# Kernel optimization log

Hardware: AMD Instinct MI355X
Metric: run time of the kernel (lower is better)

The kernel has to match this reference:

```python
import jax, jax.numpy as jnp
import numpy as np
from jax import lax

EPS = 1e-12  # tf.nn.l2_normalize epsilon


def setup_inputs() -> dict:
    key = jax.random.key(0)
    k1, k2, k3 = jax.random.split(key, 3)
    B, T, D, C, F, K = 64, 2048, 1024, 1024, 256, 5
    sentence_embed = jax.random.normal(k1, (B, T, D), dtype=jnp.float32)
    label_embed = jax.random.normal(k2, (C, D), dtype=jnp.float32)
    conv_w = jax.random.normal(k3, (K, C, F), dtype=jnp.float32) * 0.05
    conv_b = jnp.zeros((F,), dtype=jnp.float32)
    return {"sentence_embed": sentence_embed, "label_embed": label_embed,
            "conv_w": conv_w, "conv_b": conv_b}


def reference(sentence_embed, label_embed, conv_w, conv_b):
    # l2-normalize label embeddings along feature dim (tf.nn.l2_normalize semantics)
    sq = jnp.sum(label_embed * label_embed, axis=-1, keepdims=True)
    label_norm = label_embed * lax.rsqrt(jnp.maximum(sq, EPS))
    # G: [B, T, C] = sentence_embed @ label_norm^T (raw sentence_embed, per original)
    G = jnp.einsum('btd,cd->btc', sentence_embed, label_norm)
    # Conv1D over time, 'same' padding, relu: [B, T, F]
    conv = lax.conv_general_dilated(
        G, conv_w, window_strides=(1,), padding='SAME',
        dimension_numbers=('NWC', 'WIO', 'NWC'))
    conv = jax.nn.relu(conv + conv_b)
    # max over filters -> attention values [B, T] (NOT softmaxed in original output path)
    att_v = jnp.max(conv, axis=-1)
    # batch_dot(sentence_embed, att_v, axes=[1,1]) -> [B, D]
    H_enc = jnp.einsum('btd,bt->bd', sentence_embed, att_v)
    return H_enc
```

## Files before the change

kernel.cpp:

```cpp
#include <hip/hip_runtime.h>

typedef unsigned short u16;
typedef __attribute__((ext_vector_type(4))) float f32x4;
typedef __attribute__((ext_vector_type(8))) short s16x8;
typedef __attribute__((ext_vector_type(4))) unsigned short u16x4;

#define DEV __device__ __forceinline__

constexpr int Bb = 64, Tt = 2048, Dd = 1024, Cc = 1024, Ff = 256;
constexpr int TP = Tt + 4;
constexpr int M1 = Bb * Tt;

DEV u16 f2bf(float f) {
    union { float f; unsigned u; } v; v.f = f;
    unsigned r = v.u + 0x7fffu + ((v.u >> 16) & 1u);
    return (u16)(r >> 16);
}
DEV float bf2f(u16 h) {
    union { unsigned u; float f; } v; v.u = ((unsigned)h) << 16; return v.f;
}

DEV void gl_lds16(const u16* g, u16* l) {
    __builtin_amdgcn_global_load_lds(
        (const __attribute__((address_space(1))) unsigned*)(const void*)g,
        (__attribute__((address_space(3))) unsigned*)(void*)l,
        16, 0, 0);
}

DEV int swz_scol(int lane) { return (((lane & 7) ^ ((lane >> 3) & 7)) << 3); }
DEV int swz_rd(int row, int e) { return e ^ ((row & 7) << 3); }

__global__ __launch_bounds__(256) void k_s2bf(const float* __restrict__ S,
                                              u16* __restrict__ Sb) {
    size_t i = ((size_t)blockIdx.x * 256 + threadIdx.x) * 8;
    const size_t stride = (size_t)gridDim.x * 256 * 8;
    const size_t n = (size_t)M1 * Dd;
    for (; i < n; i += stride) {
        f32x4 a = *(const f32x4*)(S + i);
        f32x4 b = *(const f32x4*)(S + i + 4);
        s16x8 r;
        r[0] = (short)f2bf(a.x); r[1] = (short)f2bf(a.y);
        r[2] = (short)f2bf(a.z); r[3] = (short)f2bf(a.w);
        r[4] = (short)f2bf(b.x); r[5] = (short)f2bf(b.y);
        r[6] = (short)f2bf(b.z); r[7] = (short)f2bf(b.w);
        *(s16x8*)(Sb + i) = r;
    }
}

__global__ __launch_bounds__(256) void k_label_norm(const float* __restrict__ L,
                                                    u16* __restrict__ Ln) {
    int c = blockIdx.x;
    int t = threadIdx.x;
    const float* row = L + (size_t)c * Dd;
    float s = 0.f;
    for (int d = t; d < Dd; d += 256) { float v = row[d]; s += v * v; }
    for (int o = 32; o; o >>= 1) s += __shfl_down(s, o);
    __shared__ float red[4];
    if ((t & 63) == 0) red[t >> 6] = s;
    __syncthreads();
    float tot = red[0] + red[1] + red[2] + red[3];
    float r = rsqrtf(fmaxf(tot, 1e-12f));
    for (int d = t; d < Dd; d += 256) Ln[(size_t)c * Dd + d] = f2bf(row[d] * r);
}

__global__ __launch_bounds__(256) void k_wt(const float* __restrict__ W,
                                            u16* __restrict__ Wt) {
    __shared__ float tile[64][65];
    int k = blockIdx.x; int c0 = blockIdx.y * 64; int f0 = blockIdx.z * 64;
    int tid = threadIdx.x;
    const float* Wk = W + (size_t)k * Cc * Ff;
    #pragma unroll
    for (int i = 0; i < 16; ++i) {
        int q = tid + i * 256;
        int ci = q >> 6, fj = q & 63;
        tile[ci][fj] = Wk[(size_t)(c0 + ci) * Ff + f0 + fj];
    }
    __syncthreads();
    #pragma unroll
    for (int i = 0; i < 16; ++i) {
        int q = tid + i * 256;
        int fi = q >> 6, cj = q & 63;
        Wt[((size_t)k * Ff + f0 + fi) * Cc + c0 + cj] = f2bf(tile[cj][fi]);
    }
}

__global__ __launch_bounds__(256) void k_zpad(u16* __restrict__ Gp) {
    int b_ = blockIdx.x, tid = threadIdx.x;
    size_t base = (size_t)b_ * TP * Cc;
    for (int i = tid; i < 2 * Cc; i += 256) {
        Gp[base + i] = 0;
        Gp[base + (size_t)(TP - 2) * Cc + i] = 0;
    }
}

__global__ __launch_bounds__(512, 2) void k_gemm1_8ph(const u16* __restrict__ Sb,
                                                      const u16* __restrict__ Ln,
                                                      u16* __restrict__ Gp) {
    __shared__ alignas(16) u16 As[2][256 * 64];
    __shared__ alignas(16) u16 Bs[2][256 * 64];
    int bid = blockIdx.x;
    int xcd = bid & 7, idx = bid >> 3;
    int mt = xcd * 64 + (idx >> 2);
    int nt = idx & 3;
    const int m0 = mt * 256, n0 = nt * 256;
    int tid = threadIdx.x, lane = tid & 63, wid = tid >> 6;
    int wm = wid >> 2, wn = wid & 3;
    int srow = lane >> 3, scol = swz_scol(lane);
    const int rsel = lane & 15;
    const int klo = (lane >> 4) * 8, khi = 32 + klo;
    f32x4 acc[8][4] = {};

    auto stageA = [&](int kt, int h, int buf) {
        #pragma unroll
        for (int i = 0; i < 2; ++i) {
            int seg = h * 16 + wid * 2 + i;
            gl_lds16(Sb + (size_t)(m0 + seg * 8 + srow) * Dd + kt * 64 + scol,
                     &As[buf][seg * 512]);
        }
    };
    auto stageB = [&](int kt, int h, int buf) {
        #pragma unroll
        for (int i = 0; i < 2; ++i) {
            int seg = h * 16 + wid * 2 + i;
            gl_lds16(Ln + (size_t)(n0 + seg * 8 + srow) * Dd + kt * 64 + scol,
                     &Bs[buf][seg * 512]);
        }
    };

    stageA(0, 0, 0); stageA(0, 1, 0);
    stageB(0, 0, 0); stageB(0, 1, 0);
    asm volatile("s_waitcnt vmcnt(0)" ::: "memory");
    asm volatile("s_barrier" ::: "memory");

    for (int kt = 0; kt < 16; ++kt) {
        const int cur = kt & 1, nxt = cur ^ 1;
        const u16* Ab = As[cur];
        const u16* Bq = Bs[cur];
        s16x8 a[4], b[4];
        #pragma unroll
        for (int f = 0; f < 4; ++f) {
            int row = wm * 128 + f * 16 + rsel;
            a[f] = *(const s16x8*)&Ab[row * 64 + swz_rd(row, klo)];
        }
        #pragma unroll
        for (int f = 0; f < 4; ++f) {
            int row = wn * 64 + f * 16 + rsel;
            b[f] = *(const s16x8*)&Bq[row * 64 + swz_rd(row, klo)];
        }
        if (kt < 15) { stageA(kt + 1, 0, nxt); stageB(kt + 1, 0, nxt); }
        __builtin_amdgcn_s_barrier();
        __builtin_amdgcn_s_setprio(1);
        #pragma unroll
        for (int fm = 0; fm < 4; ++fm)
            #pragma unroll
            for (int fn = 0; fn < 4; ++fn)
                acc[fm][fn] = __builtin_amdgcn_mfma_f32_16x16x32_bf16(
                    a[fm], b[fn], acc[fm][fn], 0, 0, 0);
        __builtin_amdgcn_s_setprio(0);
        __builtin_amdgcn_s_barrier();
        #pragma unroll
        for (int f = 0; f < 4; ++f) {
            int row = wm * 128 + 64 + f * 16 + rsel;
            a[f] = *(const s16x8*)&Ab[row * 64 + swz_rd(row, klo)];
        }
        if (kt < 15) { stageA(kt + 1, 1, nxt); stageB(kt + 1, 1, nxt); }
        __builtin_amdgcn_s_barrier();
        __builtin_amdgcn_s_setprio(1);
        #pragma unroll
        for (int fm = 0; fm < 4; ++fm)
            #pragma unroll
            for (int fn = 0; fn < 4; ++fn)
                acc[4 + fm][fn] = __builtin_amdgcn_mfma_f32_16x16x32_bf16(
                    a[fm], b[fn], acc[4 + fm][fn], 0, 0, 0);
        __builtin_amdgcn_s_setprio(0);
        __builtin_amdgcn_s_barrier();
        #pragma unroll
        for (int f = 0; f < 4; ++f) {
            int row = wm * 128 + f * 16 + rsel;
            a[f] = *(const s16x8*)&Ab[row * 64 + swz_rd(row, khi)];
        }
        #pragma unroll
        for (int f = 0; f < 4; ++f) {
            int row = wn * 64 + f * 16 + rsel;
            b[f] = *(const s16x8*)&Bq[row * 64 + swz_rd(row, khi)];
        }
        __builtin_amdgcn_s_barrier();
        __builtin_amdgcn_s_setprio(1);
        #pragma unroll
        for (int fm = 0; fm < 4; ++fm)
            #pragma unroll
            for (int fn = 0; fn < 4; ++fn)
                acc[fm][fn] = __builtin_amdgcn_mfma_f32_16x16x32_bf16(
                    a[fm], b[fn], acc[fm][fn], 0, 0, 0);
        __builtin_amdgcn_s_setprio(0);
        __builtin_amdgcn_s_barrier();
        #pragma unroll
        for (int f = 0; f < 4; ++f) {
            int row = wm * 128 + 64 + f * 16 + rsel;
            a[f] = *(const s16x8*)&Ab[row * 64 + swz_rd(row, khi)];
        }
        __builtin_amdgcn_s_barrier();
        __builtin_amdgcn_s_setprio(1);
        #pragma unroll
        for (int fm = 0; fm < 4; ++fm)
            #pragma unroll
            for (int fn = 0; fn < 4; ++fn)
                acc[4 + fm][fn] = __builtin_amdgcn_mfma_f32_16x16x32_bf16(
                    a[fm], b[fn], acc[4 + fm][fn], 0, 0, 0);
        __builtin_amdgcn_s_setprio(0);
        asm volatile("s_waitcnt vmcnt(0)" ::: "memory");
        asm volatile("s_barrier" ::: "memory");
    }
    #pragma unroll
    for (int m = 0; m < 8; ++m) {
        #pragma unroll
        for (int r = 0; r < 4; ++r) {
            int row = m0 + wm * 128 + (m >> 2) * 64 + (m & 3) * 16 + (lane >> 4) * 4 + r;
            int b_ = row >> 11, t = row & 2047;
            size_t base = ((size_t)b_ * TP + t + 2) * Cc;
            #pragma unroll
            for (int n = 0; n < 4; ++n) {
                int col = n0 + wn * 64 + n * 16 + rsel;
                Gp[base + col] = f2bf(acc[m][n][r]);
            }
        }
    }
}

__global__ __launch_bounds__(256) void k_gemm1_f32(const float* __restrict__ S,
                                                   const u16* __restrict__ Ln,
                                                   u16* __restrict__ Gp) {
    __shared__ alignas(16) u16 As[128 * 64];
    __shared__ alignas(16) u16 Bs[128 * 64];
    int bid = blockIdx.x;
    int xcd = bid & 7, idx = bid >> 3;
    int mt = xcd * 128 + (idx >> 3);
    int nt = idx & 7;
    const int m0 = mt * 128, n0 = nt * 128;
    int tid = threadIdx.x;
    int lane = tid & 63, wid = tid >> 6;
    int wm = wid >> 1, wn = wid & 1;
    f32x4 acc[4][4] = {};

    for (int kt = 0; kt < 16; ++kt) {
        int k0 = kt * 64;
        #pragma unroll
        for (int i = 0; i < 8; ++i) {
            int q = tid + i * 256;
            int row = q >> 4, c4 = (q & 15) * 4;
            f32x4 v = *(const f32x4*)(S + (size_t)(m0 + row) * Dd + k0 + c4);
            u16* p = &As[row * 64 + c4];
            p[0] = f2bf(v.x); p[1] = f2bf(v.y); p[2] = f2bf(v.z); p[3] = f2bf(v.w);
        }
        #pragma unroll
        for (int i = 0; i < 4; ++i) {
            int q = tid + i * 256;
            int row = q >> 3, c8 = (q & 7) * 8;
            *(s16x8*)&Bs[row * 64 + c8] =
                *(const s16x8*)(Ln + (size_t)(n0 + row) * Dd + k0 + c8);
        }
        __syncthreads();
        #pragma unroll
        for (int kk = 0; kk < 2; ++kk) {
            int rsel = lane & 15, ksel = kk * 32 + (lane >> 4) * 8;
            s16x8 a[4], b[4];
            #pragma unroll
            for (int f = 0; f < 4; ++f)
                a[f] = *(const s16x8*)&As[(wm * 64 + f * 16 + rsel) * 64 + ksel];
            #pragma unroll
            for (int f = 0; f < 4; ++f)
                b[f] = *(const s16x8*)&Bs[(wn * 64 + f * 16 + rsel) * 64 + ksel];
            #pragma unroll
            for (int fm = 0; fm < 4; ++fm)
                #pragma unroll
                for (int fn = 0; fn < 4; ++fn)
                    acc[fm][fn] = __builtin_amdgcn_mfma_f32_16x16x32_bf16(
                        a[fm], b[fn], acc[fm][fn], 0, 0, 0);
        }
        __syncthreads();
    }
    #pragma unroll
    for (int fm = 0; fm < 4; ++fm) {
        #pragma unroll
        for (int r = 0; r < 4; ++r) {
            int row = m0 + wm * 64 + fm * 16 + (lane >> 4) * 4 + r;
            int b_ = row >> 11, t = row & 2047;
            size_t base = ((size_t)b_ * TP + t + 2) * Cc;
            #pragma unroll
            for (int fn = 0; fn < 4; ++fn) {
                int col = n0 + wn * 64 + fn * 16 + (lane & 15);
                Gp[base + col] = f2bf(acc[fm][fn][r]);
            }
        }
    }
}

__global__ __launch_bounds__(512) void k_conv(const u16* __restrict__ Gp,
                                              const u16* __restrict__ Wt,
                                              const float* __restrict__ bias,
                                              float* __restrict__ att) {
    __shared__ alignas(16) u16 As[136 * 64];
    __shared__ alignas(16) u16 Bs[256 * 64];
    __shared__ float red[4][128];
    int mt = blockIdx.x;
    int b_ = mt >> 4;
    int t0 = (mt & 15) * 128;
    int tid = threadIdx.x, lane = tid & 63, wid = tid >> 6;
    int wm = wid >> 2, wn = wid & 3;
    int srow = lane >> 3, scol = swz_scol(lane);
    f32x4 acc[4][4] = {};
    const size_t gbase = ((size_t)b_ * TP + t0) * Cc;

    for (int ct = 0; ct < 16; ++ct) {
        int c0 = ct * 64;
        for (int s = wid; s < 17; s += 8)
            gl_lds16(Gp + gbase + (size_t)(s * 8 + srow) * Cc + c0 + scol, &As[s * 512]);
        for (int k = 0; k < 5; ++k) {
            #pragma unroll
            for (int i = 0; i < 4; ++i) {
                int seg = wid * 4 + i;
                gl_lds16(Wt + ((size_t)k * Ff + seg * 8 + srow) * Cc + c0 + scol,
                         &Bs[seg * 512]);
            }
            __syncthreads();
            #pragma unroll
            for (int kk = 0; kk < 2; ++kk) {
                int rsel = lane & 15, ksel = kk * 32 + (lane >> 4) * 8;
                s16x8 a[4], b[4];
                #pragma unroll
                for (int f = 0; f < 4; ++f) {
                    int row = k + wm * 64 + f * 16 + rsel;
                    a[f] = *(const s16x8*)&As[row * 64 + swz_rd(row, ksel)];
                }
                #pragma unroll
                for (int f = 0; f < 4; ++f) {
                    int row = wn * 64 + f * 16 + rsel;
                    b[f] = *(const s16x8*)&Bs[row * 64 + swz_rd(row, ksel)];
                }
                #pragma unroll
                for (int fm = 0; fm < 4; ++fm)
                    #pragma unroll
                    for (int fn = 0; fn < 4; ++fn)
                        acc[fm][fn] = __builtin_amdgcn_mfma_f32_16x16x32_bf16(
                            a[fm], b[fn], acc[fm][fn], 0, 0, 0);
            }
            __syncthreads();
        }
    }
    float bv[4];
    #pragma unroll
    for (int fn = 0; fn < 4; ++fn)
        bv[fn] = bias[wn * 64 + fn * 16 + (lane & 15)];
    #pragma unroll
    for (int fm = 0; fm < 4; ++fm) {
        #pragma unroll
        for (int r = 0; r < 4; ++r) {
            float v = 0.f;
            #pragma unroll
            for (int fn = 0; fn < 4; ++fn)
                v = fmaxf(v, fmaxf(acc[fm][fn][r] + bv[fn], 0.f));
            #pragma unroll
            for (int m = 1; m <= 8; m <<= 1) v = fmaxf(v, __shfl_xor(v, m));
            if ((lane & 15) == 0)
                red[wn][wm * 64 + fm * 16 + (lane >> 4) * 4 + r] = v;
        }
    }
    __syncthreads();
    if (tid < 128) {
        float v = fmaxf(fmaxf(red[0][tid], red[1][tid]),
                        fmaxf(red[2][tid], red[3][tid]));
        att[(size_t)mt * 128 + tid] = v;
    }
}

__global__ __launch_bounds__(256) void k_henc_bf(const u16* __restrict__ Sb,
                                                 const float* __restrict__ att,
                                                 float* __restrict__ part) {
    int b_ = blockIdx.x, tc = blockIdx.y;
    int tid = threadIdx.x;
    int d = tid * 4;
    const u16* Sp = Sb + ((size_t)b_ * Tt + (size_t)tc * 256) * Dd + d;
    const float* ap = att + (size_t)b_ * Tt + (size_t)tc * 256;
    f32x4 acc = {};
    for (int t = 0; t < 256; ++t) {
        float a = ap[t];
        u16x4 s = *(const u16x4*)(Sp + (size_t)t * Dd);
        acc.x += bf2f(s.x) * a;
        acc.y += bf2f(s.y) * a;
        acc.z += bf2f(s.z) * a;
        acc.w += bf2f(s.w) * a;
    }
    *(f32x4*)(part + ((size_t)tc * Bb + b_) * Dd + d) = acc;
}

__global__ __launch_bounds__(256) void k_henc_f32(const float* __restrict__ S,
                                                  const float* __restrict__ att,
                                                  float* __restrict__ part) {
    int b_ = blockIdx.x, tc = blockIdx.y;
    int tid = threadIdx.x;
    int d = tid * 4;
    const float* Sp = S + ((size_t)b_ * Tt + (size_t)tc * 256) * Dd + d;
    const float* ap = att + (size_t)b_ * Tt + (size_t)tc * 256;
    f32x4 acc = {};
    for (int t = 0; t < 256; ++t) {
        float a = ap[t];
        f32x4 s = *(const f32x4*)(Sp + (size_t)t * Dd);
        acc += s * a;
    }
    *(f32x4*)(part + ((size_t)tc * Bb + b_) * Dd + d) = acc;
}

__global__ __launch_bounds__(256) void k_hred(const float* __restrict__ part,
                                              float* __restrict__ out) {
    int i = blockIdx.x * 256 + threadIdx.x;
    float s = 0.f;
    #pragma unroll
    for (int p = 0; p < 8; ++p) s += part[(size_t)p * (Bb * Dd) + i];
    out[i] = s;
}

extern "C" void kernel_launch(void* const* d_in, const int* in_sizes, int n_in,
                              void* d_out, int out_size, void* d_ws, size_t ws_size,
                              hipStream_t stream) {
    const float* S  = (const float*)d_in[0];
    const float* L  = (const float*)d_in[1];
    const float* W  = (const float*)d_in[2];
    const float* cb = (const float*)d_in[3];
    float* out = (float*)d_out;
    char* ws = (char*)d_ws;

    const size_t GP_B   = (size_t)Bb * TP * Cc * 2;
    const size_t LN_B   = (size_t)Cc * Dd * 2;
    const size_t WT_B   = (size_t)5 * Ff * Cc * 2;
    const size_t ATT_B  = (size_t)M1 * 4;
    const size_t PART_B = (size_t)8 * Bb * Dd * 4;
    const size_t SB_B   = (size_t)M1 * Dd * 2;
    u16*   Gp   = (u16*)(ws);
    u16*   Ln   = (u16*)(ws + GP_B);
    u16*   Wt   = (u16*)(ws + GP_B + LN_B);
    float* att  = (float*)(ws + GP_B + LN_B + WT_B);
    float* part = (float*)(ws + GP_B + LN_B + WT_B + ATT_B);
    u16*   Sb   = (u16*)(ws + GP_B + LN_B + WT_B + ATT_B + PART_B);
    const bool use_bf = ws_size >= GP_B + LN_B + WT_B + ATT_B + PART_B + SB_B;

    k_label_norm<<<Cc, 256, 0, stream>>>(L, Ln);
    k_wt<<<dim3(5, Cc / 64, Ff / 64), 256, 0, stream>>>(W, Wt);
    k_zpad<<<Bb, 256, 0, stream>>>(Gp);
    if (use_bf) {
        k_s2bf<<<2048, 256, 0, stream>>>(S, Sb);
        k_gemm1_8ph<<<(M1 / 256) * (Cc / 256), 512, 0, stream>>>(Sb, Ln, Gp);
    } else {
        k_gemm1_f32<<<(M1 / 128) * (Cc / 128), 256, 0, stream>>>(S, Ln, Gp);
    }
    k_conv<<<M1 / 128, 512, 0, stream>>>(Gp, Wt, cb, att);
    if (use_bf) k_henc_bf<<<dim3(Bb, 8), 256, 0, stream>>>(Sb, att, part);
    else        k_henc_f32<<<dim3(Bb, 8), 256, 0, stream>>>(S, att, part);
    k_hred<<<(Bb * Dd) / 256, 256, 0, stream>>>(part, out);
}
```

Before: 958.5 us.

## Double-buffer conv LDS loads and restage GEMM1 B tile with finer waitcnts

The conv kernel changes from a load/sync/compute loop with single LDS buffers to a software pipeline. G and weight tiles are double-buffered, and the next weight slice and next channel tile are prefetched while the current one computes, with counted vmcnt waits in place of full drains. In GEMM1 the B tile is now staged in full during the first phase, and the A row-half mapping per wave is reshuffled so the second half can be waited on partially instead of draining all loads at the end of each k-step. This aims to hide global-to-LDS latency, but it doubles LDS in the conv kernel, which may reduce occupancy, and the hand-counted vmcnt values are fragile.

```diff
diff --git a/kernel.cpp b/kernel.cpp
--- a/kernel.cpp
+++ b/kernel.cpp
@@ -6,6 +6,8 @@
 typedef __attribute__((ext_vector_type(4))) unsigned short u16x4;
 
 #define DEV __device__ __forceinline__
+#define VMW(N) asm volatile("s_waitcnt vmcnt(" #N ")" ::: "memory")
+#define BARM() asm volatile("s_barrier" ::: "memory")
 
 constexpr int Bb = 64, Tt = 2048, Dd = 1024, Cc = 1024, Ff = 256;
 constexpr int TP = Tt + 4;
@@ -110,7 +112,15 @@
     const int klo = (lane >> 4) * 8, khi = 32 + klo;
     f32x4 acc[8][4] = {};
 
-    auto stageA = [&](int kt, int h, int buf) {
+    auto stageBfull = [&](int kt, int buf) {
+        #pragma unroll
+        for (int i = 0; i < 4; ++i) {
+            int seg = wid * 4 + i;
+            gl_lds16(Ln + (size_t)(n0 + seg * 8 + srow) * Dd + kt * 64 + scol,
+                     &Bs[buf][seg * 512]);
+        }
+    };
+    auto stageAh = [&](int kt, int h, int buf) {
         #pragma unroll
         for (int i = 0; i < 2; ++i) {
             int seg = h * 16 + wid * 2 + i;
@@ -118,19 +128,10 @@
                      &As[buf][seg * 512]);
         }
     };
-    auto stageB = [&](int kt, int h, int buf) {
-        #pragma unroll
-        for (int i = 0; i < 2; ++i) {
-            int seg = h * 16 + wid * 2 + i;
-            gl_lds16(Ln + (size_t)(n0 + seg * 8 + srow) * Dd + kt * 64 + scol,
-                     &Bs[buf][seg * 512]);
-        }
-    };
-
-    stageA(0, 0, 0); stageA(0, 1, 0);
-    stageB(0, 0, 0); stageB(0, 1, 0);
-    asm volatile("s_waitcnt vmcnt(0)" ::: "memory");
-    asm volatile("s_barrier" ::: "memory");
+
+    stageBfull(0, 0); stageAh(0, 0, 0);
+    stageAh(0, 1, 0);
+    VMW(2); BARM();
 
     for (int kt = 0; kt < 16; ++kt) {
         const int cur = kt & 1, nxt = cur ^ 1;
@@ -139,7 +140,7 @@
         s16x8 a[4], b[4];
         #pragma unroll
         for (int f = 0; f < 4; ++f) {
-            int row = wm * 128 + f * 16 + rsel;
+            int row = wm * 64 + f * 16 + rsel;
             a[f] = *(const s16x8*)&Ab[row * 64 + swz_rd(row, klo)];
         }
         #pragma unroll
@@ -147,7 +148,7 @@
             int row = wn * 64 + f * 16 + rsel;
             b[f] = *(const s16x8*)&Bq[row * 64 + swz_rd(row, klo)];
         }
-        if (kt < 15) { stageA(kt + 1, 0, nxt); stageB(kt + 1, 0, nxt); }
+        if (kt < 15) { stageBfull(kt + 1, nxt); stageAh(kt + 1, 0, nxt); }
         __builtin_amdgcn_s_barrier();
         __builtin_amdgcn_s_setprio(1);
         #pragma unroll
@@ -157,13 +158,14 @@
                 acc[fm][fn] = __builtin_amdgcn_mfma_f32_16x16x32_bf16(
                     a[fm], b[fn], acc[fm][fn], 0, 0, 0);
         __builtin_amdgcn_s_setprio(0);
-        __builtin_amdgcn_s_barrier();
-        #pragma unroll
-        for (int f = 0; f < 4; ++f) {
-            int row = wm * 128 + 64 + f * 16 + rsel;
+        if (kt < 15) { VMW(6); } else { VMW(0); }
+        BARM();
+        #pragma unroll
+        for (int f = 0; f < 4; ++f) {
+            int row = 128 + wm * 64 + f * 16 + rsel;
             a[f] = *(const s16x8*)&Ab[row * 64 + swz_rd(row, klo)];
         }
-        if (kt < 15) { stageA(kt + 1, 1, nxt); stageB(kt + 1, 1, nxt); }
+        if (kt < 15) stageAh(kt + 1, 1, nxt);
         __builtin_amdgcn_s_barrier();
         __builtin_amdgcn_s_setprio(1);
         #pragma unroll
@@ -176,7 +178,7 @@
         __builtin_amdgcn_s_barrier();
         #pragma unroll
         for (int f = 0; f < 4; ++f) {
-            int row = wm * 128 + f * 16 + rsel;
+            int row = wm * 64 + f * 16 + rsel;
             a[f] = *(const s16x8*)&Ab[row * 64 + swz_rd(row, khi)];
         }
         #pragma unroll
@@ -196,7 +198,7 @@
         __builtin_amdgcn_s_barrier();
         #pragma unroll
         for (int f = 0; f < 4; ++f) {
-            int row = wm * 128 + 64 + f * 16 + rsel;
+            int row = 128 + wm * 64 + f * 16 + rsel;
             a[f] = *(const s16x8*)&Ab[row * 64 + swz_rd(row, khi)];
         }
         __builtin_amdgcn_s_barrier();
@@ -208,14 +210,13 @@
                 acc[4 + fm][fn] = __builtin_amdgcn_mfma_f32_16x16x32_bf16(
                     a[fm], b[fn], acc[4 + fm][fn], 0, 0, 0);
         __builtin_amdgcn_s_setprio(0);
-        asm volatile("s_waitcnt vmcnt(0)" ::: "memory");
-        asm volatile("s_barrier" ::: "memory");
+        VMW(2); BARM();
     }
     #pragma unroll
     for (int m = 0; m < 8; ++m) {
         #pragma unroll
         for (int r = 0; r < 4; ++r) {
-            int row = m0 + wm * 128 + (m >> 2) * 64 + (m & 3) * 16 + (lane >> 4) * 4 + r;
+            int row = m0 + (m >> 2) * 128 + wm * 64 + (m & 3) * 16 + (lane >> 4) * 4 + r;
             int b_ = row >> 11, t = row & 2047;
             size_t base = ((size_t)b_ * TP + t + 2) * Cc;
             #pragma unroll
@@ -299,8 +300,8 @@
                                               const u16* __restrict__ Wt,
                                               const float* __restrict__ bias,
                                               float* __restrict__ att) {
-    __shared__ alignas(16) u16 As[136 * 64];
-    __shared__ alignas(16) u16 Bs[256 * 64];
+    __shared__ alignas(16) u16 As[2][24 * 512];
+    __shared__ alignas(16) u16 Bs[2][256 * 64];
     __shared__ float red[4][128];
     int mt = blockIdx.x;
     int b_ = mt >> 4;
@@ -311,42 +312,79 @@
     f32x4 acc[4][4] = {};
     const size_t gbase = ((size_t)b_ * TP + t0) * Cc;
 
-    for (int ct = 0; ct < 16; ++ct) {
-        int c0 = ct * 64;
-        for (int s = wid; s < 17; s += 8)
-            gl_lds16(Gp + gbase + (size_t)(s * 8 + srow) * Cc + c0 + scol, &As[s * 512]);
-        for (int k = 0; k < 5; ++k) {
-            #pragma unroll
-            for (int i = 0; i < 4; ++i) {
-                int seg = wid * 4 + i;
-                gl_lds16(Wt + ((size_t)k * Ff + seg * 8 + srow) * Cc + c0 + scol,
-                         &Bs[seg * 512]);
+    auto stage_B = [&](int s2) {
+        int ct2 = s2 / 5, k2 = s2 % 5, buf = s2 & 1;
+        #pragma unroll
+        for (int i = 0; i < 4; ++i) {
+            int seg = wid * 4 + i;
+            gl_lds16(Wt + ((size_t)k2 * Ff + seg * 8 + srow) * Cc + ct2 * 64 + scol,
+                     &Bs[buf][seg * 512]);
+        }
+    };
+    auto stage_A = [&](int ct2) {
+        int buf = ct2 & 1;
+        #pragma unroll
+        for (int i = 0; i < 3; ++i) {
+            int seg = wid * 3 + i;
+            gl_lds16(Gp + gbase + (size_t)(seg * 8 + srow) * Cc + ct2 * 64 + scol,
+                     &As[buf][seg * 512]);
+        }
+    };
+    auto compute = [&](int cb, int ca, int k) {
+        #pragma unroll
+        for (int kk = 0; kk < 2; ++kk) {
+            int rsel = lane & 15, ksel = kk * 32 + (lane >> 4) * 8;
+            s16x8 a[4], b[4];
+            #pragma unroll
+            for (int f = 0; f < 4; ++f) {
+                int row = k + wm * 64 + f * 16 + rsel;
+                a[f] = *(const s16x8*)&As[ca][row * 64 + swz_rd(row, ksel)];
             }
-            __syncthreads();
-            #pragma unroll
-            for (int kk = 0; kk < 2; ++kk) {
-                int rsel = lane & 15, ksel = kk * 32 + (lane >> 4) * 8;
-                s16x8 a[4], b[4];
+            #pragma unroll
+            for (int f = 0; f < 4; ++f) {
+                int row = wn * 64 + f * 16 + rsel;
+                b[f] = *(const s16x8*)&Bs[cb][row * 64 + swz_rd(row, ksel)];
+            }
+            #pragma unroll
+            for (int fm = 0; fm < 4; ++fm)
                 #pragma unroll
-                for (int f = 0; f < 4; ++f) {
-                    int row = k + wm * 64 + f * 16 + rsel;
-                    a[f] = *(const s16x8*)&As[row * 64 + swz_rd(row, ksel)];
-                }
-                #pragma unroll
-                for (int f = 0; f < 4; ++f) {
-                    int row = wn * 64 + f * 16 + rsel;
-                    b[f] = *(const s16x8*)&Bs[row * 64 + swz_rd(row, ksel)];
-                }
-                #pragma unroll
-                for (int fm = 0; fm < 4; ++fm)
-                    #pragma unroll
-                    for (int fn = 0; fn < 4; ++fn)
-                        acc[fm][fn] = __builtin_amdgcn_mfma_f32_16x16x32_bf16(
-                            a[fm], b[fn], acc[fm][fn], 0, 0, 0);
-            }
-            __syncthreads();
-        }
-    }
+                for (int fn = 0; fn < 4; ++fn)
+                    acc[fm][fn] = __builtin_amdgcn_mfma_f32_16x16x32_bf16(
+                        a[fm], b[fn], acc[fm][fn], 0, 0, 0);
+        }
+    };
+
+    stage_A(0); stage_B(0); stage_B(1);
+
+    for (int ct = 0; ct < 15; ++ct) {
+        int s = ct * 5, ca = ct & 1;
+        VMW(4); BARM();
+        compute(s & 1, ca, 0);
+        BARM();
+        stage_B(s + 2); stage_A(ct + 1);
+        VMW(7); BARM();
+        compute((s + 1) & 1, ca, 1);
+        BARM();
+        stage_B(s + 3);
+        VMW(4); BARM();
+        compute((s + 2) & 1, ca, 2);
+        BARM();
+        stage_B(s + 4);
+        VMW(4); BARM();
+        compute((s + 3) & 1, ca, 3);
+        BARM();
+        stage_B(s + 5);
+        VMW(4); BARM();
+        compute((s + 4) & 1, ca, 4);
+        BARM();
+        stage_B(s + 6);
+    }
+    VMW(4); BARM(); compute(1, 1, 0); BARM(); stage_B(77);
+    VMW(4); BARM(); compute(0, 1, 1); BARM(); stage_B(78);
+    VMW(4); BARM(); compute(1, 1, 2); BARM(); stage_B(79);
+    VMW(4); BARM(); compute(0, 1, 3); BARM();
+    VMW(0); BARM(); compute(1, 1, 4); BARM();
+
     float bv[4];
     #pragma unroll
     for (int fn = 0; fn < 4; ++fn)
```

Result: faster. 897.8 us (-6.3%).
